# Optimization experiments

Measured on AMD Instinct MI355X. Metric: run time of the kernel, lower is better.

## Reference

```python
import jax, jax.numpy as jnp
import numpy as np

IMG_H, IMG_W = 1024, 1024
TWO_PI = 2.0 * np.pi


def _pe_encoding(coords_norm, gauss):
    # coords_norm: [..., 2] in [0,1]
    c = 2.0 * coords_norm - 1.0
    c = (c @ gauss) * TWO_PI  # [..., num_pos_feats]
    return jnp.concatenate([jnp.sin(c), jnp.cos(c)], axis=-1)  # [..., embed_dim]


def setup_inputs() -> dict:
    key = jax.random.key(0)
    ks = jax.random.split(key, 9)
    B, N, D = 2048, 128, 256
    points = jax.random.uniform(ks[0], (B, N, 2), dtype=jnp.float32) * 1024.0
    labels = jax.random.randint(ks[1], (B, N), -1, 2, dtype=jnp.int32)  # {-1,0,1}
    boxes = jax.random.uniform(ks[2], (B, 4), dtype=jnp.float32) * 1024.0
    gauss = jax.random.normal(ks[3], (2, D // 2), dtype=jnp.float32)  # scale=1.0
    pe0 = jax.random.normal(ks[4], (D,), dtype=jnp.float32)
    pe1 = jax.random.normal(ks[5], (D,), dtype=jnp.float32)
    pe2 = jax.random.normal(ks[6], (D,), dtype=jnp.float32)
    pe3 = jax.random.normal(ks[7], (D,), dtype=jnp.float32)
    nap = jax.random.normal(ks[8], (D,), dtype=jnp.float32)
    return {"points": points, "labels": labels, "boxes": boxes, "gauss": gauss,
            "pe0": pe0, "pe1": pe1, "pe2": pe2, "pe3": pe3, "nap": nap}


def reference(points, labels, boxes, gauss, pe0, pe1, pe2, pe3, nap):
    inv_size = jnp.asarray([1.0 / IMG_W, 1.0 / IMG_H], dtype=points.dtype)

    # --- _embed_points (pad=False since boxes are given) ---
    p = (points + 0.5) * inv_size  # normalize x by W, y by H
    point_emb = _pe_encoding(p, gauss)  # [B, N, D]
    lab = labels[..., None]  # [B, N, 1]
    delta = jnp.where(lab == -1, nap,
             jnp.where(lab == 1, pe0,
              jnp.where(lab == 0, pe1, jnp.zeros_like(nap))))
    point_emb = point_emb + delta

    # --- _embed_boxes ---
    b = (boxes + 0.5).reshape(boxes.shape[0], 2, 2) * inv_size
    corner_emb = _pe_encoding(b, gauss)  # [B, 2, D]
    corner_emb = corner_emb + jnp.stack([pe2, pe3], axis=0)  # broadcast over B
    box_emb = jnp.mean(corner_emb, axis=1, keepdims=True)  # [B, 1, D]

    combined = jnp.concatenate([point_emb, box_emb], axis=1)  # [B, N+1, D]
    return jnp.mean(combined, axis=1, keepdims=True)  # [B, 1, D]
```

## Files before the change

### kernel.cpp

```cpp
#include <hip/hip_runtime.h>
#include <math.h>


#define N_PTS 128
#define NFEAT 128

__device__ __forceinline__ float sin2pi(float t) { return __builtin_amdgcn_sinf(t); }
__device__ __forceinline__ float cos2pi(float t) { return __builtin_amdgcn_cosf(t); }
__device__ __forceinline__ float fract_(float t) { return __builtin_amdgcn_fractf(t); }

__global__ __launch_bounds__(256)
void prompt_encoder_kernel(const float* __restrict__ points,
                           const int*   __restrict__ labels,
                           const float* __restrict__ boxes,
                           const float* __restrict__ gauss,
                           const float* __restrict__ pe0,
                           const float* __restrict__ pe1,
                           const float* __restrict__ pe2,
                           const float* __restrict__ pe3,
                           const float* __restrict__ nap,
                           float* __restrict__ out)
{
    const int b   = blockIdx.x;
    const int tid = threadIdx.x;
    const int j   = tid & (NFEAT - 1);
    const int h   = tid >> 7;

    __shared__ float2 sc[N_PTS];
    __shared__ float  psin[2 * NFEAT];
    __shared__ float  pcos[2 * NFEAT];
    __shared__ int    scnt[4];

    if (tid < 4) scnt[tid] = 0;
    if (tid < N_PTS) {
        float2 p = ((const float2*)(points + (size_t)b * N_PTS * 2))[tid];
        sc[tid] = make_float2((p.x + 0.5f) * (1.0f / 512.0f) - 1.0f,
                              (p.y + 0.5f) * (1.0f / 512.0f) - 1.0f);
    }
    __syncthreads();

    if (tid < N_PTS) {
        int lab = labels[(size_t)b * N_PTS + tid];
        atomicAdd(&scnt[lab + 1], 1);
    }

    const float g0 = gauss[j];
    const float g1 = gauss[NFEAT + j];

    float ss = 0.0f, cs = 0.0f;
    const int n0 = h * (N_PTS / 2);
    #pragma unroll 8
    for (int n = 0; n < N_PTS / 2; ++n) {
        float2 c = sc[n0 + n];
        float  t = fract_(fmaf(c.x, g0, c.y * g1));
        ss += sin2pi(t);
        cs += cos2pi(t);
    }
    psin[tid] = ss;
    pcos[tid] = cs;
    __syncthreads();

    const int d  = tid;
    const int jj = d & (NFEAT - 1);
    float sum = (d < NFEAT) ? (psin[jj] + psin[NFEAT + jj])
                            : (pcos[jj] + pcos[NFEAT + jj]);

    float cm1 = (float)scnt[0];
    float c0n = (float)scnt[1];
    float cp1 = (float)scnt[2];
    float delv = cm1 * nap[d] + cp1 * pe0[d] + c0n * pe1[d];

    float gg0 = gauss[jj];
    float gg1 = gauss[NFEAT + jj];
    float4 bx = ((const float4*)boxes)[b];
    float t0 = fract_(fmaf((bx.x + 0.5f) * (1.0f / 512.0f) - 1.0f, gg0,
                           ((bx.y + 0.5f) * (1.0f / 512.0f) - 1.0f) * gg1));
    float t1 = fract_(fmaf((bx.z + 0.5f) * (1.0f / 512.0f) - 1.0f, gg0,
                           ((bx.w + 0.5f) * (1.0f / 512.0f) - 1.0f) * gg1));
    float tr0, tr1;
    if (d < NFEAT) { tr0 = sin2pi(t0); tr1 = sin2pi(t1); }
    else           { tr0 = cos2pi(t0); tr1 = cos2pi(t1); }
    float box = 0.5f * ((tr0 + pe2[d]) + (tr1 + pe3[d]));

    out[(size_t)b * 256 + d] = (sum + delv + box) * (1.0f / (float)(N_PTS + 1));
}

extern "C" void kernel_launch(void* const* d_in, const int* in_sizes, int n_in,
                              void* d_out, int out_size, void* d_ws, size_t ws_size,
                              hipStream_t stream) {
    const float* points = (const float*)d_in[0];
    const int*   labels = (const int*)d_in[1];
    const float* boxes  = (const float*)d_in[2];
    const float* gauss  = (const float*)d_in[3];
    const float* pe0    = (const float*)d_in[4];
    const float* pe1    = (const float*)d_in[5];
    const float* pe2    = (const float*)d_in[6];
    const float* pe3    = (const float*)d_in[7];
    const float* nap    = (const float*)d_in[8];
    float* out = (float*)d_out;

    const int B = in_sizes[2] / 4;

    prompt_encoder_kernel<<<B, 256, 0, stream>>>(points, labels, boxes, gauss,
                                                 pe0, pe1, pe2, pe3, nap, out);
}
```

Before: 14.51 us.

## Broadcast point coords via readlane and count labels with wave ballots

Each wave now loads its own 64 points into registers and broadcasts them with readlane (scalar operands) instead of staging normalized coordinates in shared memory. Label counting uses per-wave ballot+popcount instead of shared-memory atomics, which removes one barrier. The normalization is folded into pre-scaled gauss coefficients plus a constant, and the loop runs with two independent accumulator pairs. This changes the floating-point rounding slightly and fully unrolls 64 iterations, which raises code size.

```diff
diff --git a/kernel.cpp b/kernel.cpp
--- a/kernel.cpp
+++ b/kernel.cpp
@@ -1,13 +1,15 @@
 #include <hip/hip_runtime.h>
-#include <math.h>
 
 
+#define NFEAT 128
 #define N_PTS 128
-#define NFEAT 128
 
 __device__ __forceinline__ float sin2pi(float t) { return __builtin_amdgcn_sinf(t); }
 __device__ __forceinline__ float cos2pi(float t) { return __builtin_amdgcn_cosf(t); }
 __device__ __forceinline__ float fract_(float t) { return __builtin_amdgcn_fractf(t); }
+__device__ __forceinline__ float rdlane(float v, int l) {
+    return __int_as_float(__builtin_amdgcn_readlane(__float_as_int(v), l));
+}
 
 __global__ __launch_bounds__(256)
 void prompt_encoder_kernel(const float* __restrict__ points,
@@ -21,62 +23,69 @@
                            const float* __restrict__ nap,
                            float* __restrict__ out)
 {
-    const int b   = blockIdx.x;
-    const int tid = threadIdx.x;
-    const int j   = tid & (NFEAT - 1);
-    const int h   = tid >> 7;
+    const int b    = blockIdx.x;
+    const int tid  = threadIdx.x;
+    const int lane = tid & 63;
+    const int w    = tid >> 6;
+    const int jf   = (w & 1) * 64 + lane;
+    const int h    = w >> 1;
 
-    __shared__ float2 sc[N_PTS];
-    __shared__ float  psin[2 * NFEAT];
-    __shared__ float  pcos[2 * NFEAT];
-    __shared__ int    scnt[4];
+    __shared__ float ps[4][64];
+    __shared__ float pc[4][64];
+    __shared__ int   scnt[6];
 
-    if (tid < 4) scnt[tid] = 0;
-    if (tid < N_PTS) {
-        float2 p = ((const float2*)(points + (size_t)b * N_PTS * 2))[tid];
-        sc[tid] = make_float2((p.x + 0.5f) * (1.0f / 512.0f) - 1.0f,
-                              (p.y + 0.5f) * (1.0f / 512.0f) - 1.0f);
+    float2 p = ((const float2*)points)[(size_t)b * N_PTS + h * 64 + lane];
+
+    if (w < 2) {
+        int lab = labels[(size_t)b * N_PTS + w * 64 + lane];
+        unsigned long long bm1 = __ballot(lab == -1);
+        unsigned long long bz  = __ballot(lab == 0);
+        unsigned long long bp1 = __ballot(lab == 1);
+        if (lane == 0) {
+            scnt[w * 3 + 0] = __popcll(bm1);
+            scnt[w * 3 + 1] = __popcll(bz);
+            scnt[w * 3 + 2] = __popcll(bp1);
+        }
     }
+
+    const float a  = 1.0f / 512.0f;
+    const float g0 = gauss[jf];
+    const float g1 = gauss[NFEAT + jf];
+    const float G0 = g0 * a, G1 = g1 * a;
+    const float C  = (0.5f * a - 1.0f) * (g0 + g1);
+
+    float ss0 = 0.f, ss1 = 0.f, cs0 = 0.f, cs1 = 0.f;
+    #pragma unroll
+    for (int l = 0; l < 64; l += 2) {
+        float sx0 = rdlane(p.x, l),     sy0 = rdlane(p.y, l);
+        float sx1 = rdlane(p.x, l + 1), sy1 = rdlane(p.y, l + 1);
+        float t0 = fract_(fmaf(sx0, G0, fmaf(sy0, G1, C)));
+        float t1 = fract_(fmaf(sx1, G0, fmaf(sy1, G1, C)));
+        ss0 += sin2pi(t0); cs0 += cos2pi(t0);
+        ss1 += sin2pi(t1); cs1 += cos2pi(t1);
+    }
+    ps[w][lane] = ss0 + ss1;
+    pc[w][lane] = cs0 + cs1;
     __syncthreads();
 
-    if (tid < N_PTS) {
-        int lab = labels[(size_t)b * N_PTS + tid];
-        atomicAdd(&scnt[lab + 1], 1);
-    }
+    const int d   = tid;
+    const int j   = d & (NFEAT - 1);
+    const int wlo = j >> 6;
+    const int li  = j & 63;
+    float sum = (d < NFEAT) ? (ps[wlo][li] + ps[wlo + 2][li])
+                            : (pc[wlo][li] + pc[wlo + 2][li]);
 
-    const float g0 = gauss[j];
-    const float g1 = gauss[NFEAT + j];
-
-    float ss = 0.0f, cs = 0.0f;
-    const int n0 = h * (N_PTS / 2);
-    #pragma unroll 8
-    for (int n = 0; n < N_PTS / 2; ++n) {
-        float2 c = sc[n0 + n];
-        float  t = fract_(fmaf(c.x, g0, c.y * g1));
-        ss += sin2pi(t);
-        cs += cos2pi(t);
-    }
-    psin[tid] = ss;
-    pcos[tid] = cs;
-    __syncthreads();
-
-    const int d  = tid;
-    const int jj = d & (NFEAT - 1);
-    float sum = (d < NFEAT) ? (psin[jj] + psin[NFEAT + jj])
-                            : (pcos[jj] + pcos[NFEAT + jj]);
-
-    float cm1 = (float)scnt[0];
-    float c0n = (float)scnt[1];
-    float cp1 = (float)scnt[2];
+    float cm1 = (float)(scnt[0] + scnt[3]);
+    float c0n = (float)(scnt[1] + scnt[4]);
+    float cp1 = (float)(scnt[2] + scnt[5]);
     float delv = cm1 * nap[d] + cp1 * pe0[d] + c0n * pe1[d];
 
-    float gg0 = gauss[jj];
-    float gg1 = gauss[NFEAT + jj];
+    float gg0 = gauss[j], gg1 = gauss[NFEAT + j];
     float4 bx = ((const float4*)boxes)[b];
-    float t0 = fract_(fmaf((bx.x + 0.5f) * (1.0f / 512.0f) - 1.0f, gg0,
-                           ((bx.y + 0.5f) * (1.0f / 512.0f) - 1.0f) * gg1));
-    float t1 = fract_(fmaf((bx.z + 0.5f) * (1.0f / 512.0f) - 1.0f, gg0,
-                           ((bx.w + 0.5f) * (1.0f / 512.0f) - 1.0f) * gg1));
+    float t0 = fract_(fmaf((bx.x + 0.5f) * a - 1.0f, gg0,
+                           ((bx.y + 0.5f) * a - 1.0f) * gg1));
+    float t1 = fract_(fmaf((bx.z + 0.5f) * a - 1.0f, gg0,
+                           ((bx.w + 0.5f) * a - 1.0f) * gg1));
     float tr0, tr1;
     if (d < NFEAT) { tr0 = sin2pi(t0); tr1 = sin2pi(t1); }
     else           { tr0 = cos2pi(t0); tr1 = cos2pi(t1); }
```

New measurement: 16.50 us. 13.7% more time.
